# Performance work log

Hardware: AMD Instinct MI355X
Metric: run time of the kernel (lower is better)

Reference implementation:

```python
import jax, jax.numpy as jnp
import numpy as np

B, H, W, C = 64, 14, 14, 768

def setup_inputs() -> dict:
    key = jax.random.key(0)
    k = jax.random.split(key, 5)
    s = 0.02  # small init so tanh/sigmoid stay in active range
    return {
        "x": jax.random.normal(k[0], (B, H, W, C), dtype=jnp.float32),
        "Wx": jax.random.normal(k[1], (3 * C, C), dtype=jnp.float32) * s,
        "bx": jnp.zeros((3 * C,), dtype=jnp.float32),
        "Wh": jax.random.normal(k[2], (3 * C, C), dtype=jnp.float32) * s,
        "bh": jnp.zeros((3 * C,), dtype=jnp.float32),
        "Wp": jax.random.normal(k[3], (C, C), dtype=jnp.float32) * s,
    }

def reference(x, Wx, bx, Wh, bh, Wp):
    b, h_, w_, c = x.shape
    n = h_ * w_
    seq = x.reshape(b, n, c)
    # Input projections for all timesteps at once (no recurrent dependency).
    x_zrn = jnp.einsum('bnc,dc->bnd', seq, Wx) + bx  # [B, N, 3C]
    x_zrn_t = jnp.transpose(x_zrn, (1, 0, 2))        # [N, B, 3C] for scan

    def step(h, xz):
        h_zrn = h @ Wh.T + bh                         # [B, 3C]
        x_z, x_r, x_n = jnp.split(xz, 3, axis=-1)
        h_z, h_r, h_n = jnp.split(h_zrn, 3, axis=-1)
        z = jax.nn.sigmoid(x_z + h_z)
        r = jax.nn.sigmoid(x_r + h_r)
        ncand = jnp.tanh(x_n + r * h_n)
        h_new = (1.0 - z) * ncand + z * h
        return h_new, h_new

    h0 = jnp.zeros((b, c), dtype=x.dtype)
    _, hs = jax.lax.scan(step, h0, x_zrn_t)           # hs: [N, B, C]
    y = jnp.transpose(hs, (1, 0, 2))                  # [B, N, C]
    y = jnp.einsum('bnc,dc->bnd', y, Wp)              # proj (no bias)
    # proj_drop = 0.0 -> identity
    return y.reshape(b, h_, w_, c)
```

## Files before the change

### kernel.cpp

```cpp
#include <hip/hip_runtime.h>

typedef unsigned short u16;
typedef unsigned int   u32;
typedef unsigned long long u64;
typedef __attribute__((ext_vector_type(8))) short bf16x8;
typedef __attribute__((ext_vector_type(4))) float f32x4;

#define GK 768
#define NSTEP 196
#define NWG 96
#define CPW 8
#define RROWS 24
#define HSTEP 49152

__device__ __forceinline__ u16 f2bf(float f) {
    u32 u = __float_as_uint(f);
    u = (u + 0x7fffu + ((u >> 16) & 1u)) >> 16;
    return (u16)u;
}
__device__ __forceinline__ float bf2f(u16 h) { return __uint_as_float(((u32)h) << 16); }

__global__ __launch_bounds__(256) void cvt_kernel(
    const float4* __restrict__ x, const float4* __restrict__ wx,
    const float4* __restrict__ wp,
    u32* __restrict__ xb, u32* __restrict__ wxb, u32* __restrict__ wpb,
    int* __restrict__ flags)
{
    const int N1 = 9633792 / 4, N2 = 1769472 / 4;
    int i = blockIdx.x * 256 + threadIdx.x;
    if (blockIdx.x == 0) flags[threadIdx.x] = 0;
    const float4* src; u32* dst; int off;
    if (i < N1)            { src = x;  dst = xb;  off = i; }
    else if (i < N1 + N2)  { src = wx; dst = wxb; off = i - N1; }
    else                   { src = wp; dst = wpb; off = i - N1 - N2; }
    float4 v = src[off];
    u32 lo = (u32)f2bf(v.x) | ((u32)f2bf(v.y) << 16);
    u32 hi = (u32)f2bf(v.z) | ((u32)f2bf(v.w) << 16);
    dst[(size_t)off * 2]     = lo;
    dst[(size_t)off * 2 + 1] = hi;
}

template<int MODE>
__global__ __launch_bounds__(256) void gemm_bt(
    const u16* __restrict__ A, const u16* __restrict__ B,
    const float* __restrict__ bias, void* __restrict__ outv)
{
    __shared__ u16 As[128 * 40];
    __shared__ u16 Bs[128 * 40];
    const int tid  = threadIdx.x;
    const int lane = tid & 63;
    const int wv   = tid >> 6;
    const int m0 = blockIdx.y * 128;
    const int n0 = blockIdx.x * 128;
    const int wm = (wv & 1) * 64;
    const int wn = (wv >> 1) * 64;

    f32x4 acc[4][4];
#pragma unroll
    for (int i = 0; i < 4; ++i)
#pragma unroll
        for (int j = 0; j < 4; ++j) acc[i][j] = (f32x4){0.f, 0.f, 0.f, 0.f};

    const int r0 = tid >> 2, q0 = tid & 3;
    const u16* gA0 = A + (size_t)(m0 + r0)      * GK + q0 * 8;
    const u16* gA1 = A + (size_t)(m0 + r0 + 64) * GK + q0 * 8;
    const u16* gB0 = B + (size_t)(n0 + r0)      * GK + q0 * 8;
    const u16* gB1 = B + (size_t)(n0 + r0 + 64) * GK + q0 * 8;
    u16* sA0 = As + r0 * 40 + q0 * 8;
    u16* sA1 = As + (r0 + 64) * 40 + q0 * 8;
    u16* sB0 = Bs + r0 * 40 + q0 * 8;
    u16* sB1 = Bs + (r0 + 64) * 40 + q0 * 8;

    const int fr = lane & 15, fq = lane >> 4;
    const u16* fA = As + (wm + fr) * 40 + fq * 8;
    const u16* fB = Bs + (wn + fr) * 40 + fq * 8;

    for (int kt = 0; kt < GK / 32; ++kt) {
        uint4 a0 = *(const uint4*)(gA0 + kt * 32);
        uint4 a1 = *(const uint4*)(gA1 + kt * 32);
        uint4 b0 = *(const uint4*)(gB0 + kt * 32);
        uint4 b1 = *(const uint4*)(gB1 + kt * 32);
        __syncthreads();
        *(uint4*)sA0 = a0; *(uint4*)sA1 = a1;
        *(uint4*)sB0 = b0; *(uint4*)sB1 = b1;
        __syncthreads();
        bf16x8 af[4], bfr[4];
#pragma unroll
        for (int mi = 0; mi < 4; ++mi) af[mi]  = *(const bf16x8*)(fA + mi * 16 * 40);
#pragma unroll
        for (int ni = 0; ni < 4; ++ni) bfr[ni] = *(const bf16x8*)(fB + ni * 16 * 40);
#pragma unroll
        for (int mi = 0; mi < 4; ++mi)
#pragma unroll
            for (int ni = 0; ni < 4; ++ni)
                acc[mi][ni] = __builtin_amdgcn_mfma_f32_16x16x32_bf16(
                    af[mi], bfr[ni], acc[mi][ni], 0, 0, 0);
    }

    if (MODE == 1) {
        u16* out = (u16*)outv;
#pragma unroll
        for (int mi = 0; mi < 4; ++mi) {
#pragma unroll
            for (int ni = 0; ni < 4; ++ni) {
                int col = n0 + wn + ni * 16 + fr;
                float bv = bias[col];
#pragma unroll
                for (int r = 0; r < 4; ++r) {
                    int m = m0 + wm + mi * 16 + fq * 4 + r;
                    int b = m / 196;
                    int nn = m - b * 196;
                    u16 hv = f2bf(acc[mi][ni][r] + bv);
                    int other = __shfl_xor((int)hv, 1, 64);
                    if (!(lane & 1)) {
                        u32 packed = (u32)hv | (((u32)(u16)other) << 16);
                        size_t eidx = ((size_t)nn * 64 + (size_t)b) * 2304 + (size_t)col;
                        *((u32*)out + (eidx >> 1)) = packed;
                    }
                }
            }
        }
    } else {
        float* out = (float*)outv;
#pragma unroll
        for (int mi = 0; mi < 4; ++mi) {
#pragma unroll
            for (int ni = 0; ni < 4; ++ni) {
                int col = n0 + wn + ni * 16 + fr;
#pragma unroll
                for (int r = 0; r < 4; ++r) {
                    int m = m0 + wm + mi * 16 + fq * 4 + r;
                    int b = m & 63;
                    int nn = m >> 6;
                    out[((size_t)b * 196 + nn) * 768 + col] = acc[mi][ni][r];
                }
            }
        }
    }
}

__global__ __launch_bounds__(512) void recur_kernel(
    const u16* __restrict__ xz,
    const float* __restrict__ Wh,
    const float* __restrict__ bh,
    u16* __restrict__ hsx,
    int* flags)
{
    __shared__ float hz_s[2][64 * 28];
    __shared__ float hold_s[512];

    const int tid  = threadIdx.x;
    const int wg   = blockIdx.x;
    const int c0   = wg * CPW;
    const int lane = tid & 63;
    const int wv   = tid >> 6;
    const int mi   = wv & 3;
    const int kh   = wv >> 2;
    const int fr   = lane & 15, fq = lane >> 4;

    __builtin_amdgcn_fence(__ATOMIC_ACQUIRE, "agent");

    bf16x8 bfrag[2][12];
#pragma unroll
    for (int ni = 0; ni < 2; ++ni) {
        int row = ni * 16 + fr;
        bool valid = row < RROWS;
        int gate = row >> 3, ch = row & 7;
        const float* wp = Wh + (size_t)(valid ? (gate * 768 + c0 + ch) : 0) * 768;
#pragma unroll
        for (int kk = 0; kk < 12; ++kk) {
            int k0 = (kh * 12 + kk) * 32 + fq * 8;
            float4 f0 = *(const float4*)(wp + k0);
            float4 f1 = *(const float4*)(wp + k0 + 4);
            bf16x8 b;
            b[0] = (short)f2bf(f0.x); b[1] = (short)f2bf(f0.y);
            b[2] = (short)f2bf(f0.z); b[3] = (short)f2bf(f0.w);
            b[4] = (short)f2bf(f1.x); b[5] = (short)f2bf(f1.y);
            b[6] = (short)f2bf(f1.z); b[7] = (short)f2bf(f1.w);
            if (!valid) b = (bf16x8){0,0,0,0,0,0,0,0};
            bfrag[ni][kk] = b;
        }
    }

    hold_s[tid] = 0.f;
    __syncthreads();

    const int gb = tid >> 3, gi = tid & 7;
    const int gc = c0 + gi;
    const float bh0 = bh[gc], bh1 = bh[768 + gc], bh2 = bh[1536 + gc];

    const int aoff = (mi * 16 + fr) * 768 + kh * 384 + fq * 8;

    for (int n = 0; n < NSTEP; ++n) {
        size_t xoff = (size_t)n * 147456 + (size_t)gb * 2304 + (size_t)gc;
        float xg0 = bf2f(xz[xoff]);
        float xg1 = bf2f(xz[xoff + 768]);
        float xg2 = bf2f(xz[xoff + 1536]);

        f32x4 acc0 = (f32x4){0.f, 0.f, 0.f, 0.f};
        f32x4 acc1 = (f32x4){0.f, 0.f, 0.f, 0.f};

        if (n > 0) {
            for (;;) {
                int v0 = __hip_atomic_load(&flags[lane], __ATOMIC_RELAXED,
                                           __HIP_MEMORY_SCOPE_AGENT);
                int v1 = __hip_atomic_load(&flags[lane + 32], __ATOMIC_RELAXED,
                                           __HIP_MEMORY_SCOPE_AGENT);
                if (__all((v0 < v1 ? v0 : v1) >= n)) break;
            }

            const u16* ap = hsx + (size_t)(n - 1) * HSTEP + aoff;
#pragma unroll
            for (int kk = 0; kk < 12; ++kk) {
                bf16x8 a = *(const bf16x8*)(ap + kk * 32);
                acc0 = __builtin_amdgcn_mfma_f32_16x16x32_bf16(a, bfrag[0][kk], acc0, 0, 0, 0);
                acc1 = __builtin_amdgcn_mfma_f32_16x16x32_bf16(a, bfrag[1][kk], acc1, 0, 0, 0);
            }
        }

        {
            int bat = mi * 16 + fq * 4;
#pragma unroll
            for (int r = 0; r < 4; ++r)
                hz_s[kh][(bat + r) * 28 + fr] = acc0[r];
            if (fr < 8) {
#pragma unroll
                for (int r = 0; r < 4; ++r)
                    hz_s[kh][(bat + r) * 28 + 16 + fr] = acc1[r];
            }
        }
        __syncthreads();

        float h0 = hz_s[0][gb * 28 + gi]      + hz_s[1][gb * 28 + gi]      + bh0;
        float h1 = hz_s[0][gb * 28 + 8 + gi]  + hz_s[1][gb * 28 + 8 + gi]  + bh1;
        float h2 = hz_s[0][gb * 28 + 16 + gi] + hz_s[1][gb * 28 + 16 + gi] + bh2;
        float z  = 1.f / (1.f + __expf(-(xg0 + h0)));
        float rr = 1.f / (1.f + __expf(-(xg1 + h1)));
        float pre = xg2 + rr * h2;
        float e2 = __expf(-2.f * pre);
        float nc = (1.f - e2) / (1.f + e2);
        float hold = hold_s[tid];
        float hnew = (1.f - z) * nc + z * hold;
        hold_s[tid] = hnew;

        u16 hv = f2bf(hnew);
        u32 other = ((u32)__shfl_xor((int)hv, 1, 64)) & 0xffffu;
        u32 v01 = (u32)hv | (other << 16);
        u32 v23 = (u32)__shfl_xor((int)v01, 2, 64);
        if ((tid & 3) == 0) {
            u64 q = (u64)v01 | ((u64)v23 << 32);
            size_t ofs = (size_t)n * HSTEP + (size_t)gb * 768 + (size_t)gc;
            __hip_atomic_store((u64*)((u32*)hsx + (ofs >> 1)), q,
                               __ATOMIC_RELAXED, __HIP_MEMORY_SCOPE_AGENT);
        }
        __syncthreads();
        if (tid == 0)
            __hip_atomic_store(&flags[wg], n + 1, __ATOMIC_RELAXED,
                               __HIP_MEMORY_SCOPE_AGENT);
    }
}

extern "C" void kernel_launch(void* const* d_in, const int* in_sizes, int n_in,
                              void* d_out, int out_size, void* d_ws, size_t ws_size,
                              hipStream_t stream)
{
    const float* x  = (const float*)d_in[0];
    const float* Wx = (const float*)d_in[1];
    const float* bx = (const float*)d_in[2];
    const float* Wh = (const float*)d_in[3];
    const float* bh = (const float*)d_in[4];
    const float* Wp = (const float*)d_in[5];
    float* out = (float*)d_out;

    char* ws = (char*)d_ws;
    size_t off = 0;
    auto wsalloc = [&](size_t bytes) -> void* {
        void* p = ws + off;
        off += (bytes + 255) & ~(size_t)255;
        return p;
    };
    u16* xb   = (u16*)wsalloc(9633792ull * 2);
    u16* wxb  = (u16*)wsalloc(1769472ull * 2);
    u16* wpb  = (u16*)wsalloc(589824ull * 2);
    u16* xzrn = (u16*)wsalloc(196ull * 64 * 2304 * 2);
    u16* hsx  = (u16*)wsalloc(196ull * 64 * 768 * 2);
    int* flags = (int*)wsalloc(1024);

    cvt_kernel<<<11712, 256, 0, stream>>>(
        (const float4*)x, (const float4*)Wx, (const float4*)Wp,
        (u32*)xb, (u32*)wxb, (u32*)wpb, flags);

    gemm_bt<1><<<dim3(18, 98), 256, 0, stream>>>(xb, wxb, bx, (void*)xzrn);

    {
        const u16* a0 = xzrn; const float* a1 = Wh; const float* a2 = bh;
        u16* a3 = hsx; int* a4 = flags;
        void* args[5] = { &a0, &a1, &a2, &a3, &a4 };
        hipLaunchCooperativeKernel((void*)recur_kernel, dim3(NWG), dim3(512),
                                   args, 0, stream);
    }

    gemm_bt<0><<<dim3(6, 98), 256, 0, stream>>>(hsx, wpb, nullptr, (void*)out);
}
```

Measured before the change: 1.355 ms.

## Partition GRU recurrence by XCD with per-XCD flags and batch slices

The recurrent kernel is restructured so each workgroup reads its XCD id from a hardware register and claims a slot via a per-XCD ticket counter. Each XCD then processes its own 8-batch slice independently across 24 workgroups of 32 channels, and synchronizes only through per-XCD flags. This keeps the step-to-step spin-wait and the hidden-state exchange local to one XCD's L2 instead of spanning the whole device. It launches 256 oversubscribed workgroups with large dynamic LDS to force one per CU, and surplus workgroups exit. It relies on the assumption that every XCD receives at least 24 workgroups, otherwise it deadlocks.

Result: no change. 1.363 ms (+0.6%).

```diff
diff --git a/kernel.cpp b/kernel.cpp
--- a/kernel.cpp
+++ b/kernel.cpp
@@ -8,10 +8,12 @@
 
 #define GK 768
 #define NSTEP 196
-#define NWG 96
-#define CPW 8
-#define RROWS 24
 #define HSTEP 49152
+#define NWG2 256
+#define WPX 24
+#define CPW2 32
+#define THR2 384
+#define DYNLDS 82000
 
 __device__ __forceinline__ u16 f2bf(float f) {
     u32 u = __float_as_uint(f);
@@ -24,11 +26,12 @@
     const float4* __restrict__ x, const float4* __restrict__ wx,
     const float4* __restrict__ wp,
     u32* __restrict__ xb, u32* __restrict__ wxb, u32* __restrict__ wpb,
-    int* __restrict__ flags)
+    int* __restrict__ flagmem)
 {
     const int N1 = 9633792 / 4, N2 = 1769472 / 4;
     int i = blockIdx.x * 256 + threadIdx.x;
-    if (blockIdx.x == 0) flags[threadIdx.x] = 0;
+    if (blockIdx.x == 0) flagmem[threadIdx.x] = 0;
+    else if (blockIdx.x == 1 && threadIdx.x < 64) flagmem[256 + threadIdx.x] = 0;
     const float4* src; u32* dst; int off;
     if (i < N1)            { src = x;  dst = xb;  off = i; }
     else if (i < N1 + N2)  { src = wx; dst = wxb; off = i - N1; }
@@ -139,123 +142,131 @@
     }
 }
 
-__global__ __launch_bounds__(512) void recur_kernel(
+__global__ __launch_bounds__(THR2) void recur2_kernel(
     const u16* __restrict__ xz,
     const float* __restrict__ Wh,
     const float* __restrict__ bh,
     u16* __restrict__ hsx,
-    int* flags)
+    int* flagmem)
 {
-    __shared__ float hz_s[2][64 * 28];
-    __shared__ float hold_s[512];
-
-    const int tid  = threadIdx.x;
-    const int wg   = blockIdx.x;
-    const int c0   = wg * CPW;
+    extern __shared__ char smem[];
+    float* hz = (float*)smem;
+    int*   mb = (int*)(smem + 3200);
+
+    const int tid = threadIdx.x;
+    int* flags   = flagmem;
+    int* tickets = flagmem + 256;
+
+    if (tid == 0) {
+        int x = __builtin_amdgcn_s_getreg(6164) & 7;
+        int s = __hip_atomic_fetch_add(&tickets[x], 1, __ATOMIC_RELAXED,
+                                       __HIP_MEMORY_SCOPE_AGENT);
+        mb[0] = x; mb[1] = s;
+    }
+    __syncthreads();
+    const int xcd = mb[0], slot = mb[1];
+    if (slot >= WPX) return;
+
     const int lane = tid & 63;
     const int wv   = tid >> 6;
-    const int mi   = wv & 3;
-    const int kh   = wv >> 2;
     const int fr   = lane & 15, fq = lane >> 4;
-
-    __builtin_amdgcn_fence(__ATOMIC_ACQUIRE, "agent");
-
-    bf16x8 bfrag[2][12];
-#pragma unroll
-    for (int ni = 0; ni < 2; ++ni) {
-        int row = ni * 16 + fr;
-        bool valid = row < RROWS;
-        int gate = row >> 3, ch = row & 7;
-        const float* wp = Wh + (size_t)(valid ? (gate * 768 + c0 + ch) : 0) * 768;
-#pragma unroll
-        for (int kk = 0; kk < 12; ++kk) {
-            int k0 = (kh * 12 + kk) * 32 + fq * 8;
-            float4 f0 = *(const float4*)(wp + k0);
-            float4 f1 = *(const float4*)(wp + k0 + 4);
+    const int c0   = slot * CPW2;
+
+    bf16x8 bfrag[24];
+    {
+        int R = wv * 16 + fr;
+        int gate = R >> 5, ch = R & 31;
+        const float* wp = Wh + (size_t)(gate * 768 + c0 + ch) * 768 + fq * 8;
+#pragma unroll
+        for (int kk = 0; kk < 24; ++kk) {
+            float4 f0 = *(const float4*)(wp + kk * 32);
+            float4 f1 = *(const float4*)(wp + kk * 32 + 4);
             bf16x8 b;
             b[0] = (short)f2bf(f0.x); b[1] = (short)f2bf(f0.y);
             b[2] = (short)f2bf(f0.z); b[3] = (short)f2bf(f0.w);
             b[4] = (short)f2bf(f1.x); b[5] = (short)f2bf(f1.y);
             b[6] = (short)f2bf(f1.z); b[7] = (short)f2bf(f1.w);
-            if (!valid) b = (bf16x8){0,0,0,0,0,0,0,0};
-            bfrag[ni][kk] = b;
-        }
-    }
-
-    hold_s[tid] = 0.f;
-    __syncthreads();
-
-    const int gb = tid >> 3, gi = tid & 7;
-    const int gc = c0 + gi;
-    const float bh0 = bh[gc], bh1 = bh[768 + gc], bh2 = bh[1536 + gc];
-
-    const int aoff = (mi * 16 + fr) * 768 + kh * 384 + fq * 8;
+            bfrag[kk] = b;
+        }
+    }
+
+    int gbatch = 0, gc = 0;
+    float bh0 = 0.f, bh1 = 0.f, bh2 = 0.f;
+    const int gb = (tid >> 5) & 7, gch = tid & 31;
+    if (tid < 256) {
+        gc = c0 + gch;
+        gbatch = xcd * 8 + gb;
+        bh0 = bh[gc]; bh1 = bh[768 + gc]; bh2 = bh[1536 + gc];
+    }
+    float hold = 0.f;
+
+    const int aoff = (xcd * 8 + (fr & 7)) * 768 + fq * 8;
 
     for (int n = 0; n < NSTEP; ++n) {
-        size_t xoff = (size_t)n * 147456 + (size_t)gb * 2304 + (size_t)gc;
-        float xg0 = bf2f(xz[xoff]);
-        float xg1 = bf2f(xz[xoff + 768]);
-        float xg2 = bf2f(xz[xoff + 1536]);
-
-        f32x4 acc0 = (f32x4){0.f, 0.f, 0.f, 0.f};
-        f32x4 acc1 = (f32x4){0.f, 0.f, 0.f, 0.f};
+        float xg0 = 0.f, xg1 = 0.f, xg2 = 0.f;
+        if (tid < 256) {
+            size_t xoff = (size_t)n * 147456 + (size_t)gbatch * 2304 + (size_t)gc;
+            xg0 = bf2f(xz[xoff]);
+            xg1 = bf2f(xz[xoff + 768]);
+            xg2 = bf2f(xz[xoff + 1536]);
+        }
+
+        f32x4 accA = (f32x4){0.f, 0.f, 0.f, 0.f};
+        f32x4 accB = (f32x4){0.f, 0.f, 0.f, 0.f};
 
         if (n > 0) {
+            int* fl = flags + xcd * 32;
             for (;;) {
-                int v0 = __hip_atomic_load(&flags[lane], __ATOMIC_RELAXED,
-                                           __HIP_MEMORY_SCOPE_AGENT);
-                int v1 = __hip_atomic_load(&flags[lane + 32], __ATOMIC_RELAXED,
-                                           __HIP_MEMORY_SCOPE_AGENT);
-                if (__all((v0 < v1 ? v0 : v1) >= n)) break;
+                int v = 0x7fffffff;
+                if (lane < WPX)
+                    v = __hip_atomic_load(&fl[lane], __ATOMIC_RELAXED,
+                                          __HIP_MEMORY_SCOPE_AGENT);
+                if (__all(v >= n)) break;
             }
 
             const u16* ap = hsx + (size_t)(n - 1) * HSTEP + aoff;
 #pragma unroll
             for (int kk = 0; kk < 12; ++kk) {
-                bf16x8 a = *(const bf16x8*)(ap + kk * 32);
-                acc0 = __builtin_amdgcn_mfma_f32_16x16x32_bf16(a, bfrag[0][kk], acc0, 0, 0, 0);
-                acc1 = __builtin_amdgcn_mfma_f32_16x16x32_bf16(a, bfrag[1][kk], acc1, 0, 0, 0);
-            }
-        }
-
-        {
-            int bat = mi * 16 + fq * 4;
+                union { uint4 u; bf16x8 v; } a0, a1;
+                a0.u = *(const uint4*)(ap + kk * 32);
+                a1.u = *(const uint4*)(ap + (kk + 12) * 32);
+                accA = __builtin_amdgcn_mfma_f32_16x16x32_bf16(a0.v, bfrag[kk], accA, 0, 0, 0);
+                accB = __builtin_amdgcn_mfma_f32_16x16x32_bf16(a1.v, bfrag[kk + 12], accB, 0, 0, 0);
+            }
+        }
+
+        if (fq < 2) {
 #pragma unroll
             for (int r = 0; r < 4; ++r)
-                hz_s[kh][(bat + r) * 28 + fr] = acc0[r];
-            if (fr < 8) {
-#pragma unroll
-                for (int r = 0; r < 4; ++r)
-                    hz_s[kh][(bat + r) * 28 + 16 + fr] = acc1[r];
-            }
+                hz[(wv * 16 + fr) * 8 + fq * 4 + r] = accA[r] + accB[r];
         }
         __syncthreads();
 
-        float h0 = hz_s[0][gb * 28 + gi]      + hz_s[1][gb * 28 + gi]      + bh0;
-        float h1 = hz_s[0][gb * 28 + 8 + gi]  + hz_s[1][gb * 28 + 8 + gi]  + bh1;
-        float h2 = hz_s[0][gb * 28 + 16 + gi] + hz_s[1][gb * 28 + 16 + gi] + bh2;
-        float z  = 1.f / (1.f + __expf(-(xg0 + h0)));
-        float rr = 1.f / (1.f + __expf(-(xg1 + h1)));
-        float pre = xg2 + rr * h2;
-        float e2 = __expf(-2.f * pre);
-        float nc = (1.f - e2) / (1.f + e2);
-        float hold = hold_s[tid];
-        float hnew = (1.f - z) * nc + z * hold;
-        hold_s[tid] = hnew;
-
-        u16 hv = f2bf(hnew);
-        u32 other = ((u32)__shfl_xor((int)hv, 1, 64)) & 0xffffu;
-        u32 v01 = (u32)hv | (other << 16);
-        u32 v23 = (u32)__shfl_xor((int)v01, 2, 64);
-        if ((tid & 3) == 0) {
-            u64 q = (u64)v01 | ((u64)v23 << 32);
-            size_t ofs = (size_t)n * HSTEP + (size_t)gb * 768 + (size_t)gc;
-            __hip_atomic_store((u64*)((u32*)hsx + (ofs >> 1)), q,
-                               __ATOMIC_RELAXED, __HIP_MEMORY_SCOPE_AGENT);
+        if (tid < 256) {
+            float h0 = hz[gch * 8 + gb]        + bh0;
+            float h1 = hz[(32 + gch) * 8 + gb] + bh1;
+            float h2 = hz[(64 + gch) * 8 + gb] + bh2;
+            float z  = 1.f / (1.f + __expf(-(xg0 + h0)));
+            float rr = 1.f / (1.f + __expf(-(xg1 + h1)));
+            float pre = xg2 + rr * h2;
+            float e2 = __expf(-2.f * pre);
+            float nc = (1.f - e2) / (1.f + e2);
+            float hnew = (1.f - z) * nc + z * hold;
+            hold = hnew;
+
+            u16 hv = f2bf(hnew);
+            u32 p  = (u32)hv | (((u32)__shfl_xor((int)hv, 1, 64) & 0xffffu) << 16);
+            u32 q  = (u32)__shfl_xor((int)p, 2, 64);
+            u32 r0 = (u32)__shfl_xor((int)p, 4, 64);
+            u32 r1 = (u32)__shfl_xor((int)q, 4, 64);
+            if ((gch & 7) == 0) {
+                uint4 val; val.x = p; val.y = q; val.z = r0; val.w = r1;
+                *(uint4*)(hsx + (size_t)n * HSTEP + (size_t)gbatch * 768 + gc) = val;
+            }
         }
         __syncthreads();
         if (tid == 0)
-            __hip_atomic_store(&flags[wg], n + 1, __ATOMIC_RELAXED,
+            __hip_atomic_store(&flags[xcd * 32 + slot], n + 1, __ATOMIC_RELAXED,
                                __HIP_MEMORY_SCOPE_AGENT);
     }
 }
@@ -284,20 +295,23 @@
     u16* wpb  = (u16*)wsalloc(589824ull * 2);
     u16* xzrn = (u16*)wsalloc(196ull * 64 * 2304 * 2);
     u16* hsx  = (u16*)wsalloc(196ull * 64 * 768 * 2);
-    int* flags = (int*)wsalloc(1024);
+    int* flagmem = (int*)wsalloc(320 * 4);
+
+    (void)hipFuncSetAttribute((const void*)recur2_kernel,
+                              hipFuncAttributeMaxDynamicSharedMemorySize, 163840);
 
     cvt_kernel<<<11712, 256, 0, stream>>>(
         (const float4*)x, (const float4*)Wx, (const float4*)Wp,
-        (u32*)xb, (u32*)wxb, (u32*)wpb, flags);
+        (u32*)xb, (u32*)wxb, (u32*)wpb, flagmem);
 
     gemm_bt<1><<<dim3(18, 98), 256, 0, stream>>>(xb, wxb, bx, (void*)xzrn);
 
     {
         const u16* a0 = xzrn; const float* a1 = Wh; const float* a2 = bh;
-        u16* a3 = hsx; int* a4 = flags;
+        u16* a3 = hsx; int* a4 = flagmem;
         void* args[5] = { &a0, &a1, &a2, &a3, &a4 };
-        hipLaunchCooperativeKernel((void*)recur_kernel, dim3(NWG), dim3(512),
-                                   args, 0, stream);
+        hipLaunchCooperativeKernel((void*)recur2_kernel, dim3(NWG2), dim3(THR2),
+                                   args, DYNLDS, stream);
     }
 
     gemm_bt<0><<<dim3(6, 98), 256, 0, stream>>>(hsx, wpb, nullptr, (void*)out);
```
